# Performance work log

Measured on AMD Instinct MI355X. Metric: run time of the kernel, lower is better.

The kernel has to match this reference:

```python
import jax, jax.numpy as jnp
import numpy as np

E, H, L = 512, 512, 1   # emb_size, hidden_size, num_layers
B, S, T = 64, 1024, 256  # batch, src_len, trg_len
SCALE = 0.02


def setup_inputs() -> dict:
    key = jax.random.key(0)
    ks = jax.random.split(key, 12)
    f32 = jnp.float32
    return {
        # forward args
        "trg_embed": jax.random.normal(ks[0], (B, T, E), f32),
        "encoder_hidden": jax.random.normal(ks[1], (B, S, 2 * H), f32),
        "encoder_final": jax.random.normal(ks[2], (L, B, 2 * H), f32),
        "src_mask": jnp.ones((B, 1, S), jnp.bool_),
        "trg_mask": jnp.ones((B, 1, T), jnp.bool_),
        # Bahdanau attention params
        "W_key": jax.random.normal(ks[3], (H, 2 * H), f32) * SCALE,
        "W_query": jax.random.normal(ks[4], (H, H), f32) * SCALE,
        "v_energy": jax.random.normal(ks[5], (H,), f32) * SCALE,
        # bridge (2H -> H, with bias)
        "W_bridge": jax.random.normal(ks[6], (H, 2 * H), f32) * SCALE,
        "b_bridge": jnp.zeros((H,), f32),
        # GRU (single layer), gate order r,z,n as in torch
        "W_ih": jax.random.normal(ks[7], (3 * H, E + 2 * H), f32) * SCALE,
        "W_hh": jax.random.normal(ks[8], (3 * H, H), f32) * SCALE,
        "b_ih": jnp.zeros((3 * H,), f32),
        "b_hh": jnp.zeros((3 * H,), f32),
        # pre_output_layer: (H + 2H + E) -> H, no bias
        "W_pre": jax.random.normal(ks[9], (H, H + 2 * H + E), f32) * SCALE,
    }


def _gru_cell(x, h, W_ih, W_hh, b_ih, b_hh):
    # x: [B, E+2H], h: [B, H]; torch GRUCell math, gates r,z,n
    gi = x @ W_ih.T + b_ih
    gh = h @ W_hh.T + b_hh
    i_r, i_z, i_n = jnp.split(gi, 3, axis=-1)
    h_r, h_z, h_n = jnp.split(gh, 3, axis=-1)
    r = jax.nn.sigmoid(i_r + h_r)
    z = jax.nn.sigmoid(i_z + h_z)
    n = jnp.tanh(i_n + r * h_n)
    return (1.0 - z) * n + z * h


def reference(trg_embed, encoder_hidden, encoder_final, src_mask, trg_mask,
              W_key, W_query, v_energy, W_bridge, b_bridge,
              W_ih, W_hh, b_ih, b_hh, W_pre):
    # init_hidden: tanh(bridge(encoder_final))  -> [L, B, H]
    hidden0 = jnp.tanh(jnp.einsum('lbd,hd->lbh', encoder_final, W_bridge) + b_bridge)
    # precomputed attention keys: [B, S, H]
    proj_key = jnp.einsum('bsd,hd->bsh', encoder_hidden, W_key)
    mask = src_mask[:, 0, :]  # [B, S]
    neg = jnp.finfo(trg_embed.dtype).min

    def step(hidden, prev_embed):  # hidden [L,B,H], prev_embed [B,E]
        q = hidden[-1] @ W_query.T                       # [B, H]
        e = jnp.tanh(q[:, None, :] + proj_key)           # [B, S, H]
        scores = jnp.einsum('bsh,h->bs', e, v_energy)    # [B, S]
        scores = jnp.where(mask, scores, neg)
        alphas = jax.nn.softmax(scores, axis=-1)         # [B, S]
        context = jnp.einsum('bs,bsd->bd', alphas, encoder_hidden)  # [B, 2H]
        x = jnp.concatenate([prev_embed, context], axis=-1)         # [B, E+2H]
        h_new = _gru_cell(x, hidden[-1], W_ih, W_hh, b_ih, b_hh)    # [B, H]
        pre = jnp.concatenate([prev_embed, h_new, context], axis=-1) @ W_pre.T  # [B, H]
        return h_new[None, :, :], (h_new, pre)

    hidden_final, (outs, pres) = jax.lax.scan(step, hidden0, jnp.swapaxes(trg_embed, 0, 1))
    decoder_states = jnp.swapaxes(outs, 0, 1)        # [B, T, H]
    pre_output_vectors = jnp.swapaxes(pres, 0, 1)    # [B, T, H]
    return decoder_states, hidden_final, pre_output_vectors
```

## Files before the change

kernel.cpp:

```cpp
#include <hip/hip_runtime.h>


typedef __attribute__((ext_vector_type(8))) short bf16x8;
typedef __attribute__((ext_vector_type(4))) float f32x4;
typedef __attribute__((ext_vector_type(2))) float f32x2;
typedef unsigned short u16;
typedef unsigned char u8;
typedef unsigned int u32;

constexpr int NB = 64, NS = 1024, NT = 256, NE = 512, NH = 512, NH2 = 1024, NG3 = 1536;

#define MFMA16(a, b, c) __builtin_amdgcn_mfma_f32_16x16x32_bf16((a), (b), (c), 0, 0, 0)

__device__ __forceinline__ float bf2f(u16 u) { return __uint_as_float(((u32)u) << 16); }
__device__ __forceinline__ u16 f2bf(float f) {
    u32 u = __float_as_uint(f);
    u += 0x7FFFu + ((u >> 16) & 1u);
    return (u16)(u >> 16);
}
__device__ __forceinline__ float fast_tanh(float x) {
    float t = __expf(2.0f * x);
    return 1.0f - __fdividef(2.0f, t + 1.0f);
}
__device__ __forceinline__ float fast_sig(float x) {
    return __fdividef(1.0f, 1.0f + __expf(-x));
}

__global__ void k_cast(const float* __restrict__ src, u16* __restrict__ dst, int n4) {
    int i = blockIdx.x * blockDim.x + threadIdx.x;
    int stride = gridDim.x * blockDim.x;
    for (; i < n4; i += stride) {
        float4 v = reinterpret_cast<const float4*>(src)[i];
        ushort4 o;
        o.x = f2bf(v.x); o.y = f2bf(v.y); o.z = f2bf(v.z); o.w = f2bf(v.w);
        reinterpret_cast<ushort4*>(dst)[i] = o;
    }
}
__global__ void k_cast8(const float* __restrict__ src, u32* __restrict__ dst, int n8) {
    int i = blockIdx.x * blockDim.x + threadIdx.x;
    int stride = gridDim.x * blockDim.x;
    for (; i < n8; i += stride) {
        float4 a = reinterpret_cast<const float4*>(src)[i * 2];
        float4 b = reinterpret_cast<const float4*>(src)[i * 2 + 1];
        int w0 = 0, w1 = 0;
        w0 = __builtin_amdgcn_cvt_pk_fp8_f32(a.x, a.y, w0, false);
        w0 = __builtin_amdgcn_cvt_pk_fp8_f32(a.z, a.w, w0, true);
        w1 = __builtin_amdgcn_cvt_pk_fp8_f32(b.x, b.y, w1, false);
        w1 = __builtin_amdgcn_cvt_pk_fp8_f32(b.z, b.w, w1, true);
        uint2 o; o.x = (u32)w0; o.y = (u32)w1;
        reinterpret_cast<uint2*>(dst)[i] = o;
    }
}

__global__ __launch_bounds__(256) void k_pkgemm8(
    const float* __restrict__ A, const u16* __restrict__ Bm, u8* __restrict__ Out8) {
    __shared__ u16 As[128][72];
    __shared__ u16 Bs[128][72];
    const int mt = blockIdx.x, nt = blockIdx.y;
    const int tid = threadIdx.x, lane = tid & 63, wv = tid >> 6;
    const int m0 = mt * 128, n0 = nt * 128;
    const f32x4 fz = {0.f, 0.f, 0.f, 0.f};
    f32x4 acc[2][8];
#pragma unroll
    for (int i = 0; i < 2; ++i)
#pragma unroll
        for (int jj = 0; jj < 8; ++jj) acc[i][jj] = fz;

    for (int kt = 0; kt < 16; ++kt) {
        const int k0 = kt * 64;
        __syncthreads();
#pragma unroll
        for (int r = 0; r < 4; ++r) {
            int cc = tid + 256 * r;
            int row = cc >> 3, kc = (cc & 7) * 8;
            const float* ap = &A[(size_t)(m0 + row) * NH2 + k0 + kc];
            float4 f0 = *(const float4*)ap;
            float4 f1 = *(const float4*)(ap + 4);
            u16 hh[8] = {f2bf(f0.x), f2bf(f0.y), f2bf(f0.z), f2bf(f0.w),
                         f2bf(f1.x), f2bf(f1.y), f2bf(f1.z), f2bf(f1.w)};
            *(bf16x8*)&As[row][kc] = *(bf16x8*)hh;
            *(bf16x8*)&Bs[row][kc] = *(const bf16x8*)&Bm[(size_t)(n0 + row) * NH2 + k0 + kc];
        }
        __syncthreads();
#pragma unroll
        for (int ks = 0; ks < 2; ++ks) {
            const int kk = ks * 32 + (lane >> 4) * 8;
            bf16x8 a0 = *(const bf16x8*)&As[wv * 32 + (lane & 15)][kk];
            bf16x8 a1 = *(const bf16x8*)&As[wv * 32 + 16 + (lane & 15)][kk];
#pragma unroll
            for (int jj = 0; jj < 8; ++jj) {
                bf16x8 bb = *(const bf16x8*)&Bs[jj * 16 + (lane & 15)][kk];
                acc[0][jj] = MFMA16(a0, bb, acc[0][jj]);
                acc[1][jj] = MFMA16(a1, bb, acc[1][jj]);
            }
        }
    }
#pragma unroll
    for (int i = 0; i < 2; ++i)
#pragma unroll
        for (int jj = 0; jj < 8; ++jj)
#pragma unroll
            for (int r = 0; r < 4; ++r) {
                int m = m0 + wv * 32 + i * 16 + (lane >> 4) * 4 + r;
                int n = n0 + jj * 16 + (lane & 15);
                int pk = __builtin_amdgcn_cvt_pk_fp8_f32(acc[i][jj][r], acc[i][jj][r], 0, false);
                Out8[(size_t)m * NH + n] = (u8)(pk & 0xFF);
            }
}

__global__ __launch_bounds__(256) void k_bridge(
    const float* __restrict__ ef, const float* __restrict__ Wb, const float* __restrict__ bb,
    float* __restrict__ hf, u16* __restrict__ hbb) {
    __shared__ float efs[NH2];
    const int b = blockIdx.x, tid = threadIdx.x;
    for (int i = tid; i < NH2; i += 256) efs[i] = ef[(size_t)b * NH2 + i];
    __syncthreads();
    for (int j = tid; j < NH; j += 256) {
        float acc = bb[j];
        const float4* wr = (const float4*)&Wb[(size_t)j * NH2];
#pragma unroll 4
        for (int d4 = 0; d4 < 256; ++d4) {
            float4 w = wr[d4];
            acc += w.x * efs[d4 * 4] + w.y * efs[d4 * 4 + 1] + w.z * efs[d4 * 4 + 2] + w.w * efs[d4 * 4 + 3];
        }
        float h0 = tanhf(acc);
        hf[(size_t)b * NH + j] = h0;
        hbb[(size_t)b * NH + j] = f2bf(h0);
    }
}

__global__ __launch_bounds__(256, 4) void k_attn(
    const u8* __restrict__ pk8, const u8* __restrict__ eh8,
    const float* __restrict__ qb, const float* __restrict__ ven,
    u16* __restrict__ ctxp, float* __restrict__ denp) {
    __shared__ float wts[128];
    __shared__ float wden[4];
    __shared__ float part[128][17];
    const int b = blockIdx.x >> 3, c = blockIdx.x & 7;
    const int tid = threadIdx.x, lane = tid & 63, wv = tid >> 6;
    const int sl = lane & 3, ch = lane >> 2;
    const int h0 = ch * 32;
    const float C = 2.8853900817779268f;
    float qv2[32], vvm2[32];
    float vs = 0.f;
#pragma unroll
    for (int i4 = 0; i4 < 8; ++i4) {
        float4 q4 = *(const float4*)&qb[(size_t)b * NH + h0 + i4 * 4];
        float4 v4 = *(const float4*)&ven[h0 + i4 * 4];
        qv2[i4 * 4 + 0] = C * q4.x; qv2[i4 * 4 + 1] = C * q4.y;
        qv2[i4 * 4 + 2] = C * q4.z; qv2[i4 * 4 + 3] = C * q4.w;
        vvm2[i4 * 4 + 0] = -2.f * v4.x; vvm2[i4 * 4 + 1] = -2.f * v4.y;
        vvm2[i4 * 4 + 2] = -2.f * v4.z; vvm2[i4 * 4 + 3] = -2.f * v4.w;
        vs += v4.x + v4.y + v4.z + v4.w;
    }
#pragma unroll
    for (int off = 32; off; off >>= 1) vs += __shfl_xor(vs, off, 64);
    vs *= 0.25f;

    const u8* pkbase = pk8 + ((size_t)b * NS + c * 128 + wv * 32 + sl) * NH + h0;
    u32 pA[8], pB[8];
    *(uint4*)&pA[0] = *(const uint4*)pkbase;
    *(uint4*)&pA[4] = *(const uint4*)(pkbase + 16);
    float accg[8];
#pragma unroll
    for (int g = 0; g < 8; ++g) {
        if (g < 7) {
            const u8* nrow = pkbase + (size_t)(g + 1) * 4 * NH;
            *(uint4*)&pB[0] = *(const uint4*)nrow;
            *(uint4*)&pB[4] = *(const uint4*)(nrow + 16);
        }
        float acc0 = 0.f, acc1 = 0.f;
#pragma unroll
        for (int w = 0; w < 8; ++w) {
            f32x2 lo = __builtin_amdgcn_cvt_pk_f32_fp8(pA[w], false);
            f32x2 hi = __builtin_amdgcn_cvt_pk_f32_fp8(pA[w], true);
            const int i = w * 4;
            float x0 = __builtin_fmaf(lo[0], C, qv2[i + 0]);
            float x1 = __builtin_fmaf(lo[1], C, qv2[i + 1]);
            float x2 = __builtin_fmaf(hi[0], C, qv2[i + 2]);
            float x3 = __builtin_fmaf(hi[1], C, qv2[i + 3]);
            acc0 = __builtin_fmaf(vvm2[i + 0], __builtin_amdgcn_rcpf(__builtin_amdgcn_exp2f(x0) + 1.0f), acc0);
            acc1 = __builtin_fmaf(vvm2[i + 1], __builtin_amdgcn_rcpf(__builtin_amdgcn_exp2f(x1) + 1.0f), acc1);
            acc0 = __builtin_fmaf(vvm2[i + 2], __builtin_amdgcn_rcpf(__builtin_amdgcn_exp2f(x2) + 1.0f), acc0);
            acc1 = __builtin_fmaf(vvm2[i + 3], __builtin_amdgcn_rcpf(__builtin_amdgcn_exp2f(x3) + 1.0f), acc1);
        }
        accg[g] = acc0 + acc1;
#pragma unroll
        for (int w = 0; w < 8; ++w) pA[w] = pB[w];
    }
#pragma unroll
    for (int off = 4; off <= 32; off <<= 1) {
#pragma unroll
        for (int g = 0; g < 8; ++g) accg[g] += __shfl_xor(accg[g], off, 64);
    }
    float den_acc = 0.f;
#pragma unroll
    for (int g = 0; g < 8; ++g) {
        float w = __expf(accg[g] + vs);
        if (lane < 4) wts[wv * 32 + g * 4 + lane] = w;
        den_acc += w;
    }
#pragma unroll
    for (int off = 32; off; off >>= 1) den_acc += __shfl_xor(den_acc, off, 64);
    if (lane == 0) wden[wv] = den_acc * 0.0625f;
    __syncthreads();
    if (tid == 0) denp[c * 64 + b] = wden[0] + wden[1] + wden[2] + wden[3];

    const int half = tid >> 7, tt = tid & 127;
    const u8* ebase = eh8 + ((size_t)b * NS + c * 128 + half * 64) * NH2 + tt * 8;
    float ar[8] = {0.f, 0.f, 0.f, 0.f, 0.f, 0.f, 0.f, 0.f};
#pragma unroll 8
    for (int s = 0; s < 64; ++s) {
        float w = wts[half * 64 + s];
        uint2 uu = *(const uint2*)&ebase[(size_t)s * NH2];
        f32x2 p0 = __builtin_amdgcn_cvt_pk_f32_fp8(uu.x, false);
        f32x2 p1 = __builtin_amdgcn_cvt_pk_f32_fp8(uu.x, true);
        f32x2 p2 = __builtin_amdgcn_cvt_pk_f32_fp8(uu.y, false);
        f32x2 p3 = __builtin_amdgcn_cvt_pk_f32_fp8(uu.y, true);
        ar[0] = __builtin_fmaf(w, p0[0], ar[0]); ar[1] = __builtin_fmaf(w, p0[1], ar[1]);
        ar[2] = __builtin_fmaf(w, p1[0], ar[2]); ar[3] = __builtin_fmaf(w, p1[1], ar[3]);
        ar[4] = __builtin_fmaf(w, p2[0], ar[4]); ar[5] = __builtin_fmaf(w, p2[1], ar[5]);
        ar[6] = __builtin_fmaf(w, p3[0], ar[6]); ar[7] = __builtin_fmaf(w, p3[1], ar[7]);
    }
#pragma unroll
    for (int k = 0; k < 8; ++k) part[tt][half * 8 + k] = ar[k];
    __syncthreads();
    const int row = tid >> 1, col = (tid & 1) * 4;
    ushort4 o;
    o.x = f2bf(part[row][col + 0] + part[row][8 + col + 0]);
    o.y = f2bf(part[row][col + 1] + part[row][8 + col + 1]);
    o.z = f2bf(part[row][col + 2] + part[row][8 + col + 2]);
    o.w = f2bf(part[row][col + 3] + part[row][8 + col + 3]);
    *(ushort4*)&ctxp[((size_t)c * 64 + b) * NH2 + tid * 4] = o;
}

__global__ __launch_bounds__(256) void k_gru(
    const u16* __restrict__ teb, const u16* __restrict__ ctxp, const float* __restrict__ denp,
    const u16* __restrict__ hb_in,
    const u16* __restrict__ Wihb, const u16* __restrict__ Whhb,
    const float* __restrict__ bih, const float* __restrict__ bhh,
    const float* __restrict__ hf_in, float* __restrict__ hf_out, u16* __restrict__ hb_out,
    u16* __restrict__ hall, u16* __restrict__ ctxall,
    float* __restrict__ out_ds, float* __restrict__ out_hf, int t) {
    __shared__ u16 ctx[16][1032];
    __shared__ float pbuf[3][3][16][17];
    const int tid = threadIdx.x, lane = tid & 63, wv = tid >> 6;
    const int jt = blockIdx.x >> 2, mh = blockIdx.x & 3;
    const int jj = lane & 15;
    const int j = jt * 16 + jj;
    const int kg = lane >> 4;
    const int mrow = mh * 16 + jj;

    {
        const int r = tid >> 4;
        const int bg = mh * 16 + r;
        const int d0 = (tid & 15) * 64;
        float den = 0.f;
#pragma unroll
        for (int cc = 0; cc < 8; ++cc) den += denp[cc * 64 + bg];
        const float rd = 1.0f / den;
#pragma unroll 2
        for (int dd = 0; dd < 64; dd += 8) {
            float ac[8] = {0.f, 0.f, 0.f, 0.f, 0.f, 0.f, 0.f, 0.f};
#pragma unroll
            for (int cc = 0; cc < 8; ++cc) {
                bf16x8 v = *(const bf16x8*)&ctxp[((size_t)cc * 64 + bg) * NH2 + d0 + dd];
#pragma unroll
                for (int k = 0; k < 8; ++k) ac[k] += bf2f((u16)v[k]);
            }
            u16 o[8];
#pragma unroll
            for (int k = 0; k < 8; ++k) o[k] = f2bf(ac[k] * rd);
            *(bf16x8*)&ctx[r][d0 + dd] = *(bf16x8*)o;
        }
    }
    __syncthreads();

    const f32x4 fz = {0.f, 0.f, 0.f, 0.f};
    f32x4 g0 = fz, g1 = fz, g2 = fz;
    const u16* wr = Wihb + (size_t)j * NG3;
    const u16* wz = wr + (size_t)NH * NG3;
    const u16* wn = wr + (size_t)NH2 * NG3;
    float ho[4], bset[6];

    if (wv == 0) {
        const u16* ta = teb + ((size_t)mrow * NT + t) * NE;
#pragma unroll 4
        for (int kt = 0; kt < 16; ++kt) {
            int k0 = kt * 32 + kg * 8;
            bf16x8 a = *(const bf16x8*)&ta[k0];
            g0 = MFMA16(a, *(const bf16x8*)&wr[k0], g0);
            g1 = MFMA16(a, *(const bf16x8*)&wz[k0], g1);
            g2 = MFMA16(a, *(const bf16x8*)&wn[k0], g2);
        }
        bset[0] = bih[j]; bset[1] = bih[NH + j]; bset[2] = bih[NH2 + j];
        bset[3] = bhh[j]; bset[4] = bhh[NH + j]; bset[5] = bhh[NH2 + j];
#pragma unroll
        for (int r = 0; r < 4; ++r) ho[r] = hf_in[(size_t)(mh * 16 + kg * 4 + r) * NH + j];
    } else if (wv == 1) {
        const u16* ha = hb_in + (size_t)mrow * NH;
        const u16* vr = Whhb + (size_t)j * NH;
        const u16* vz = vr + (size_t)NH * NH;
        const u16* vn = vr + (size_t)NH2 * NH;
#pragma unroll 4
        for (int kt = 0; kt < 16; ++kt) {
            int k0 = kt * 32 + kg * 8;
            bf16x8 a = *(const bf16x8*)&ha[k0];
            g0 = MFMA16(a, *(const bf16x8*)&vr[k0], g0);
            g1 = MFMA16(a, *(const bf16x8*)&vz[k0], g1);
            g2 = MFMA16(a, *(const bf16x8*)&vn[k0], g2);
        }
#pragma unroll
        for (int r = 0; r < 4; ++r) {
            int ml = kg * 4 + r;
            pbuf[0][0][ml][jj] = g0[r];
            pbuf[1][0][ml][jj] = g1[r];
            pbuf[2][0][ml][jj] = g2[r];
        }
    } else {
        const int koff = (wv - 2) * 512;
#pragma unroll 4
        for (int kt = 0; kt < 16; ++kt) {
            int kc = koff + kt * 32 + kg * 8;
            bf16x8 a = *(const bf16x8*)&ctx[jj][kc];
            g0 = MFMA16(a, *(const bf16x8*)&wr[NE + kc], g0);
            g1 = MFMA16(a, *(const bf16x8*)&wz[NE + kc], g1);
            g2 = MFMA16(a, *(const bf16x8*)&wn[NE + kc], g2);
        }
        const int src = wv - 1;
#pragma unroll
        for (int r = 0; r < 4; ++r) {
            int ml = kg * 4 + r;
            pbuf[0][src][ml][jj] = g0[r];
            pbuf[1][src][ml][jj] = g1[r];
            pbuf[2][src][ml][jj] = g2[r];
        }
    }
    __syncthreads();

    if (wv == 0) {
#pragma unroll
        for (int r = 0; r < 4; ++r) {
            int ml = kg * 4 + r;
            int m = mh * 16 + ml;
            float gir = g0[r] + pbuf[0][1][ml][jj] + pbuf[0][2][ml][jj] + bset[0];
            float giz = g1[r] + pbuf[1][1][ml][jj] + pbuf[1][2][ml][jj] + bset[1];
            float gin = g2[r] + pbuf[2][1][ml][jj] + pbuf[2][2][ml][jj] + bset[2];
            float rr = fast_sig(gir + pbuf[0][0][ml][jj] + bset[3]);
            float zz = fast_sig(giz + pbuf[1][0][ml][jj] + bset[4]);
            float nn = fast_tanh(gin + rr * (pbuf[2][0][ml][jj] + bset[5]));
            float hn = (1.f - zz) * nn + zz * ho[r];
            u16 hb = f2bf(hn);
            hf_out[(size_t)m * NH + j] = hn;
            hb_out[(size_t)m * NH + j] = hb;
            hall[((size_t)m * NT + t) * NH + j] = hb;
            __builtin_nontemporal_store(hn, &out_ds[((size_t)m * NT + t) * NH + j]);
            if (t == NT - 1) out_hf[(size_t)m * NH + j] = hn;
        }
    } else if (wv == 1 && jt == 0) {
        const int r2 = lane >> 2;
        const int dq = (lane & 3) * 256;
        u16* dst = &ctxall[((size_t)(mh * 16 + r2) * NT + t) * NH2 + dq];
#pragma unroll 4
        for (int dd = 0; dd < 256; dd += 8)
            *(bf16x8*)&dst[dd] = *(const bf16x8*)&ctx[r2][dq + dd];
    }
}

__global__ __launch_bounds__(256) void k_q(
    const u16* __restrict__ hbn, const u16* __restrict__ Wqb, float* __restrict__ qbuf) {
    const int tid = threadIdx.x, lane = tid & 63, wv = tid >> 6;
    const int mrow = wv * 16 + (lane & 15);
    const int kg = lane >> 4;
    const int n = blockIdx.x * 16 + (lane & 15);
    const f32x4 fz = {0.f, 0.f, 0.f, 0.f};
    f32x4 aq = fz;
    const u16* ha = hbn + (size_t)mrow * NH;
    const u16* wq = Wqb + (size_t)n * NH;
#pragma unroll 4
    for (int kt = 0; kt < 16; ++kt) {
        int k0 = kt * 32 + kg * 8;
        aq = MFMA16(*(const bf16x8*)&ha[k0], *(const bf16x8*)&wq[k0], aq);
    }
#pragma unroll
    for (int r = 0; r < 4; ++r) {
        int m = wv * 16 + kg * 4 + r;
        qbuf[(size_t)m * NH + n] = aq[r];
    }
}

__global__ __launch_bounds__(256) void k_preb(
    const u16* __restrict__ teb, const u16* __restrict__ hall, const u16* __restrict__ ctxall,
    const u16* __restrict__ Wpreb, float* __restrict__ out_pre) {
    __shared__ u16 As[128][72];
    __shared__ u16 Bs[128][72];
    const int mt = blockIdx.x, nt = blockIdx.y;
    const int tid = threadIdx.x, lane = tid & 63, wv = tid >> 6;
    const int m0 = mt * 128, n0 = nt * 128;
    const f32x4 fz = {0.f, 0.f, 0.f, 0.f};
    f32x4 acc[2][8];
#pragma unroll
    for (int i = 0; i < 2; ++i)
#pragma unroll
        for (int jj = 0; jj < 8; ++jj) acc[i][jj] = fz;

    for (int kt = 0; kt < 32; ++kt) {
        const int k0 = kt * 64;
        const u16* Abase; int astride, acol;
        if (k0 < 512)       { Abase = teb;    astride = 512;  acol = k0; }
        else if (k0 < 1024) { Abase = hall;   astride = 512;  acol = k0 - 512; }
        else                { Abase = ctxall; astride = 1024; acol = k0 - 1024; }
        __syncthreads();
#pragma unroll
        for (int r = 0; r < 4; ++r) {
            int cc = tid + 256 * r;
            int row = cc >> 3, kc = (cc & 7) * 8;
            *(bf16x8*)&As[row][kc] = *(const bf16x8*)&Abase[(size_t)(m0 + row) * astride + acol + kc];
            *(bf16x8*)&Bs[row][kc] = *(const bf16x8*)&Wpreb[(size_t)(n0 + row) * 2048 + k0 + kc];
        }
        __syncthreads();
#pragma unroll
        for (int ks = 0; ks < 2; ++ks) {
            const int kk = ks * 32 + (lane >> 4) * 8;
            bf16x8 a0 = *(const bf16x8*)&As[wv * 32 + (lane & 15)][kk];
            bf16x8 a1 = *(const bf16x8*)&As[wv * 32 + 16 + (lane & 15)][kk];
#pragma unroll
            for (int jj = 0; jj < 8; ++jj) {
                bf16x8 bb = *(const bf16x8*)&Bs[jj * 16 + (lane & 15)][kk];
                acc[0][jj] = MFMA16(a0, bb, acc[0][jj]);
                acc[1][jj] = MFMA16(a1, bb, acc[1][jj]);
            }
        }
    }
#pragma unroll
    for (int i = 0; i < 2; ++i)
#pragma unroll
        for (int jj = 0; jj < 8; ++jj)
#pragma unroll
            for (int r = 0; r < 4; ++r) {
                int m = m0 + wv * 32 + i * 16 + (lane >> 4) * 4 + r;
                int n = n0 + jj * 16 + (lane & 15);
                __builtin_nontemporal_store(acc[i][jj][r], &out_pre[(size_t)m * NH + n]);
            }
}

extern "C" void kernel_launch(void* const* d_in, const int* in_sizes, int n_in,
                              void* d_out, int out_size, void* d_ws, size_t ws_size,
                              hipStream_t stream) {
    const float* trg_embed  = (const float*)d_in[0];
    const float* enc_hidden = (const float*)d_in[1];
    const float* enc_final  = (const float*)d_in[2];
    const float* W_key    = (const float*)d_in[5];
    const float* W_query  = (const float*)d_in[6];
    const float* v_energy = (const float*)d_in[7];
    const float* W_bridge = (const float*)d_in[8];
    const float* b_bridge = (const float*)d_in[9];
    const float* W_ih     = (const float*)d_in[10];
    const float* W_hh     = (const float*)d_in[11];
    const float* b_ih     = (const float*)d_in[12];
    const float* b_hh     = (const float*)d_in[13];
    const float* W_pre    = (const float*)d_in[14];

    if (ws_size < 180000000ULL) return;
    size_t off = 0;
    auto take = [&](size_t bytes) {
        void* p = (char*)d_ws + off;
        off += (bytes + 255) & ~(size_t)255;
        return p;
    };
    u8*    eh8   = (u8*)take((size_t)NB * NS * NH2);
    u8*    pk8   = (u8*)take((size_t)NB * NS * NH);
    u16*   teb   = (u16*)take((size_t)NB * NT * NE * 2);
    u16*   ctxall= (u16*)take((size_t)NB * NT * NH2 * 2);
    u16*   hall  = (u16*)take((size_t)NB * NT * NH * 2);
    u16*   Wihb  = (u16*)take((size_t)NG3 * NG3 * 2);
    u16*   Whhb  = (u16*)take((size_t)NG3 * NH * 2);
    u16*   Wpreb = (u16*)take((size_t)NH * 2048 * 2);
    u16*   Wqb   = (u16*)take((size_t)NH * NH * 2);
    u16*   Wkb   = (u16*)take((size_t)NH * NH2 * 2);
    float* hf0   = (float*)take((size_t)NB * NH * 4);
    float* hf1   = (float*)take((size_t)NB * NH * 4);
    u16*   hb0   = (u16*)take((size_t)NB * NH * 2);
    u16*   hb1   = (u16*)take((size_t)NB * NH * 2);
    float* qbuf  = (float*)take((size_t)NB * NH * 4);
    u16*   ctxp  = (u16*)take((size_t)8 * NB * NH2 * 2);
    float* denp  = (float*)take((size_t)8 * NB * 4);

    float* out_ds  = (float*)d_out;
    float* out_hf  = out_ds + (size_t)NB * NT * NH;
    float* out_pre = out_hf + (size_t)NB * NH;

    auto cast = [&](const float* src, u16* dst, int n) {
        int n4 = n / 4;
        int grid = (n4 + 255) / 256; if (grid > 2048) grid = 2048;
        k_cast<<<grid, 256, 0, stream>>>(src, dst, n4);
    };
    k_cast8<<<2048, 256, 0, stream>>>(enc_hidden, (u32*)eh8, NB * NS * NH2 / 8);
    cast(trg_embed,  teb, NB * NT * NE);
    cast(W_ih,  Wihb,  NG3 * NG3);
    cast(W_hh,  Whhb,  NG3 * NH);
    cast(W_pre, Wpreb, NH * 2048);
    cast(W_query, Wqb, NH * NH);
    cast(W_key,  Wkb,  NH * NH2);
    k_pkgemm8<<<dim3(512, 4), 256, 0, stream>>>(enc_hidden, Wkb, pk8);
    k_bridge<<<NB, 256, 0, stream>>>(enc_final, W_bridge, b_bridge, hf0, hb0);
    k_q<<<32, 256, 0, stream>>>(hb0, Wqb, qbuf);

    for (int t = 0; t < NT; ++t) {
        float* hf_in  = (t & 1) ? hf1 : hf0;
        float* hf_out = (t & 1) ? hf0 : hf1;
        u16*   hb_in  = (t & 1) ? hb1 : hb0;
        u16*   hb_out = (t & 1) ? hb0 : hb1;
        k_attn<<<NB * 8, 256, 0, stream>>>(pk8, eh8, qbuf, v_energy, ctxp, denp);
        k_gru<<<128, 256, 0, stream>>>(teb, ctxp, denp, hb_in, Wihb, Whhb, b_ih, b_hh,
                                       hf_in, hf_out, hb_out, hall, ctxall,
                                       out_ds, out_hf, t);
        k_q<<<32, 256, 0, stream>>>(hb_out, Wqb, qbuf);
    }
    k_preb<<<dim3(128, 4), 256, 0, stream>>>(teb, hall, ctxall, Wpreb, out_pre);
}
```

Measured before the change: 11.60 ms.

## Split attention into 16 source chunks and GRU into 8-row batch tiles

k_attn now uses 16 blocks per batch row, each covering 64 source positions, so the launch grows from 512 to 1024 blocks. The context reduction is restructured so each thread handles 16 columns over 16 positions, followed by a 4-way partial sum. k_gru runs 256 blocks with 8 batch rows each, which leaves half of each MFMA tile's rows idle. The softmax normalization is moved so it is applied after the context matmul. The aim is more parallelism on the per-step critical path, at the cost of more partial-context traffic and wasted MFMA work.

```diff
diff --git a/kernel.cpp b/kernel.cpp
--- a/kernel.cpp
+++ b/kernel.cpp
@@ -133,10 +133,10 @@
     const u8* __restrict__ pk8, const u8* __restrict__ eh8,
     const float* __restrict__ qb, const float* __restrict__ ven,
     u16* __restrict__ ctxp, float* __restrict__ denp) {
-    __shared__ float wts[128];
+    __shared__ float wts[64];
     __shared__ float wden[4];
-    __shared__ float part[128][17];
-    const int b = blockIdx.x >> 3, c = blockIdx.x & 7;
+    __shared__ float part[64][4][17];
+    const int b = blockIdx.x >> 4, c = blockIdx.x & 15;
     const int tid = threadIdx.x, lane = tid & 63, wv = tid >> 6;
     const int sl = lane & 3, ch = lane >> 2;
     const int h0 = ch * 32;
@@ -157,14 +157,14 @@
     for (int off = 32; off; off >>= 1) vs += __shfl_xor(vs, off, 64);
     vs *= 0.25f;
 
-    const u8* pkbase = pk8 + ((size_t)b * NS + c * 128 + wv * 32 + sl) * NH + h0;
+    const u8* pkbase = pk8 + ((size_t)b * NS + c * 64 + wv * 16 + sl) * NH + h0;
     u32 pA[8], pB[8];
     *(uint4*)&pA[0] = *(const uint4*)pkbase;
     *(uint4*)&pA[4] = *(const uint4*)(pkbase + 16);
-    float accg[8];
-#pragma unroll
-    for (int g = 0; g < 8; ++g) {
-        if (g < 7) {
+    float accg[4];
+#pragma unroll
+    for (int g = 0; g < 4; ++g) {
+        if (g < 3) {
             const u8* nrow = pkbase + (size_t)(g + 1) * 4 * NH;
             *(uint4*)&pB[0] = *(const uint4*)nrow;
             *(uint4*)&pB[4] = *(const uint4*)(nrow + 16);
@@ -191,13 +191,13 @@
 #pragma unroll
     for (int off = 4; off <= 32; off <<= 1) {
 #pragma unroll
-        for (int g = 0; g < 8; ++g) accg[g] += __shfl_xor(accg[g], off, 64);
+        for (int g = 0; g < 4; ++g) accg[g] += __shfl_xor(accg[g], off, 64);
     }
     float den_acc = 0.f;
 #pragma unroll
-    for (int g = 0; g < 8; ++g) {
+    for (int g = 0; g < 4; ++g) {
         float w = __expf(accg[g] + vs);
-        if (lane < 4) wts[wv * 32 + g * 4 + lane] = w;
+        if (lane < 4) wts[wv * 16 + g * 4 + lane] = w;
         den_acc += w;
     }
 #pragma unroll
@@ -206,31 +206,41 @@
     __syncthreads();
     if (tid == 0) denp[c * 64 + b] = wden[0] + wden[1] + wden[2] + wden[3];
 
-    const int half = tid >> 7, tt = tid & 127;
-    const u8* ebase = eh8 + ((size_t)b * NS + c * 128 + half * 64) * NH2 + tt * 8;
-    float ar[8] = {0.f, 0.f, 0.f, 0.f, 0.f, 0.f, 0.f, 0.f};
-#pragma unroll 8
-    for (int s = 0; s < 64; ++s) {
-        float w = wts[half * 64 + s];
-        uint2 uu = *(const uint2*)&ebase[(size_t)s * NH2];
-        f32x2 p0 = __builtin_amdgcn_cvt_pk_f32_fp8(uu.x, false);
-        f32x2 p1 = __builtin_amdgcn_cvt_pk_f32_fp8(uu.x, true);
-        f32x2 p2 = __builtin_amdgcn_cvt_pk_f32_fp8(uu.y, false);
-        f32x2 p3 = __builtin_amdgcn_cvt_pk_f32_fp8(uu.y, true);
-        ar[0] = __builtin_fmaf(w, p0[0], ar[0]); ar[1] = __builtin_fmaf(w, p0[1], ar[1]);
-        ar[2] = __builtin_fmaf(w, p1[0], ar[2]); ar[3] = __builtin_fmaf(w, p1[1], ar[3]);
-        ar[4] = __builtin_fmaf(w, p2[0], ar[4]); ar[5] = __builtin_fmaf(w, p2[1], ar[5]);
-        ar[6] = __builtin_fmaf(w, p3[0], ar[6]); ar[7] = __builtin_fmaf(w, p3[1], ar[7]);
-    }
-#pragma unroll
-    for (int k = 0; k < 8; ++k) part[tt][half * 8 + k] = ar[k];
+    const int qd = tid >> 6, tt = tid & 63;
+    const int d0 = tt * 16;
+    const u8* ebase = eh8 + ((size_t)b * NS + c * 64 + qd * 16) * NH2 + d0;
+    float ar[16];
+#pragma unroll
+    for (int k = 0; k < 16; ++k) ar[k] = 0.f;
+#pragma unroll 4
+    for (int s = 0; s < 16; ++s) {
+        float w = wts[qd * 16 + s];
+        uint4 uu = *(const uint4*)&ebase[(size_t)s * NH2];
+        const u32 ww[4] = {uu.x, uu.y, uu.z, uu.w};
+#pragma unroll
+        for (int q = 0; q < 4; ++q) {
+            f32x2 plo = __builtin_amdgcn_cvt_pk_f32_fp8(ww[q], false);
+            f32x2 phi = __builtin_amdgcn_cvt_pk_f32_fp8(ww[q], true);
+            ar[q * 4 + 0] = __builtin_fmaf(w, plo[0], ar[q * 4 + 0]);
+            ar[q * 4 + 1] = __builtin_fmaf(w, plo[1], ar[q * 4 + 1]);
+            ar[q * 4 + 2] = __builtin_fmaf(w, phi[0], ar[q * 4 + 2]);
+            ar[q * 4 + 3] = __builtin_fmaf(w, phi[1], ar[q * 4 + 3]);
+        }
+    }
+#pragma unroll
+    for (int k = 0; k < 16; ++k) part[tt][qd][k] = ar[k];
     __syncthreads();
-    const int row = tid >> 1, col = (tid & 1) * 4;
+    const int st = tid >> 2, k0 = (tid & 3) * 4;
+    float o0 = 0.f, o1 = 0.f, o2 = 0.f, o3 = 0.f;
+#pragma unroll
+    for (int q = 0; q < 4; ++q) {
+        o0 += part[st][q][k0 + 0];
+        o1 += part[st][q][k0 + 1];
+        o2 += part[st][q][k0 + 2];
+        o3 += part[st][q][k0 + 3];
+    }
     ushort4 o;
-    o.x = f2bf(part[row][col + 0] + part[row][8 + col + 0]);
-    o.y = f2bf(part[row][col + 1] + part[row][8 + col + 1]);
-    o.z = f2bf(part[row][col + 2] + part[row][8 + col + 2]);
-    o.w = f2bf(part[row][col + 3] + part[row][8 + col + 3]);
+    o.x = f2bf(o0); o.y = f2bf(o1); o.z = f2bf(o2); o.w = f2bf(o3);
     *(ushort4*)&ctxp[((size_t)c * 64 + b) * NH2 + tid * 4] = o;
 }
 
@@ -242,36 +252,39 @@
     const float* __restrict__ hf_in, float* __restrict__ hf_out, u16* __restrict__ hb_out,
     u16* __restrict__ hall, u16* __restrict__ ctxall,
     float* __restrict__ out_ds, float* __restrict__ out_hf, int t) {
-    __shared__ u16 ctx[16][1032];
+    __shared__ u16 ctx[8][1032];
     __shared__ float pbuf[3][3][16][17];
+    __shared__ float rden[8];
     const int tid = threadIdx.x, lane = tid & 63, wv = tid >> 6;
-    const int jt = blockIdx.x >> 2, mh = blockIdx.x & 3;
+    const int jt = blockIdx.x >> 3, mh = blockIdx.x & 7;
     const int jj = lane & 15;
     const int j = jt * 16 + jj;
     const int kg = lane >> 4;
-    const int mrow = mh * 16 + jj;
-
+    const int mrow = mh * 8 + (jj & 7);
+
+    if (tid < 8) {
+        float den = 0.f;
+#pragma unroll
+        for (int cc = 0; cc < 16; ++cc) den += denp[cc * 64 + mh * 8 + tid];
+        rden[tid] = 1.0f / den;
+    }
     {
-        const int r = tid >> 4;
-        const int bg = mh * 16 + r;
-        const int d0 = (tid & 15) * 64;
-        float den = 0.f;
-#pragma unroll
-        for (int cc = 0; cc < 8; ++cc) den += denp[cc * 64 + bg];
-        const float rd = 1.0f / den;
-#pragma unroll 2
-        for (int dd = 0; dd < 64; dd += 8) {
+        const int r = tid >> 5;
+        const int bg = mh * 8 + r;
+        const int dcol = (tid & 31) * 32;
+#pragma unroll
+        for (int dd = 0; dd < 32; dd += 8) {
             float ac[8] = {0.f, 0.f, 0.f, 0.f, 0.f, 0.f, 0.f, 0.f};
 #pragma unroll
-            for (int cc = 0; cc < 8; ++cc) {
-                bf16x8 v = *(const bf16x8*)&ctxp[((size_t)cc * 64 + bg) * NH2 + d0 + dd];
+            for (int cc = 0; cc < 16; ++cc) {
+                bf16x8 v = *(const bf16x8*)&ctxp[((size_t)cc * 64 + bg) * NH2 + dcol + dd];
 #pragma unroll
                 for (int k = 0; k < 8; ++k) ac[k] += bf2f((u16)v[k]);
             }
             u16 o[8];
 #pragma unroll
-            for (int k = 0; k < 8; ++k) o[k] = f2bf(ac[k] * rd);
-            *(bf16x8*)&ctx[r][d0 + dd] = *(bf16x8*)o;
+            for (int k = 0; k < 8; ++k) o[k] = f2bf(ac[k]);
+            *(bf16x8*)&ctx[r][dcol + dd] = *(bf16x8*)o;
         }
     }
     __syncthreads();
@@ -296,7 +309,10 @@
         bset[0] = bih[j]; bset[1] = bih[NH + j]; bset[2] = bih[NH2 + j];
         bset[3] = bhh[j]; bset[4] = bhh[NH + j]; bset[5] = bhh[NH2 + j];
 #pragma unroll
-        for (int r = 0; r < 4; ++r) ho[r] = hf_in[(size_t)(mh * 16 + kg * 4 + r) * NH + j];
+        for (int r = 0; r < 4; ++r) {
+            int ml = kg * 4 + r;
+            ho[r] = (ml < 8) ? hf_in[(size_t)(mh * 8 + ml) * NH + j] : 0.f;
+        }
     } else if (wv == 1) {
         const u16* ha = hb_in + (size_t)mrow * NH;
         const u16* vr = Whhb + (size_t)j * NH;
@@ -322,7 +338,7 @@
 #pragma unroll 4
         for (int kt = 0; kt < 16; ++kt) {
             int kc = koff + kt * 32 + kg * 8;
-            bf16x8 a = *(const bf16x8*)&ctx[jj][kc];
+            bf16x8 a = *(const bf16x8*)&ctx[jj & 7][kc];
             g0 = MFMA16(a, *(const bf16x8*)&wr[NE + kc], g0);
             g1 = MFMA16(a, *(const bf16x8*)&wz[NE + kc], g1);
             g2 = MFMA16(a, *(const bf16x8*)&wn[NE + kc], g2);
@@ -342,10 +358,12 @@
 #pragma unroll
         for (int r = 0; r < 4; ++r) {
             int ml = kg * 4 + r;
-            int m = mh * 16 + ml;
-            float gir = g0[r] + pbuf[0][1][ml][jj] + pbuf[0][2][ml][jj] + bset[0];
-            float giz = g1[r] + pbuf[1][1][ml][jj] + pbuf[1][2][ml][jj] + bset[1];
-            float gin = g2[r] + pbuf[2][1][ml][jj] + pbuf[2][2][ml][jj] + bset[2];
+            if (ml >= 8) continue;
+            int m = mh * 8 + ml;
+            float rd = rden[ml];
+            float gir = g0[r] + (pbuf[0][1][ml][jj] + pbuf[0][2][ml][jj]) * rd + bset[0];
+            float giz = g1[r] + (pbuf[1][1][ml][jj] + pbuf[1][2][ml][jj]) * rd + bset[1];
+            float gin = g2[r] + (pbuf[2][1][ml][jj] + pbuf[2][2][ml][jj]) * rd + bset[2];
             float rr = fast_sig(gir + pbuf[0][0][ml][jj] + bset[3]);
             float zz = fast_sig(giz + pbuf[1][0][ml][jj] + bset[4]);
             float nn = fast_tanh(gin + rr * (pbuf[2][0][ml][jj] + bset[5]));
@@ -358,12 +376,18 @@
             if (t == NT - 1) out_hf[(size_t)m * NH + j] = hn;
         }
     } else if (wv == 1 && jt == 0) {
-        const int r2 = lane >> 2;
-        const int dq = (lane & 3) * 256;
-        u16* dst = &ctxall[((size_t)(mh * 16 + r2) * NT + t) * NH2 + dq];
-#pragma unroll 4
-        for (int dd = 0; dd < 256; dd += 8)
-            *(bf16x8*)&dst[dd] = *(const bf16x8*)&ctx[r2][dq + dd];
+        const int r2 = lane >> 3;
+        const int dq = (lane & 7) * 128;
+        const float rd = rden[r2];
+        u16* dst = &ctxall[((size_t)(mh * 8 + r2) * NT + t) * NH2 + dq];
+#pragma unroll 4
+        for (int dd = 0; dd < 128; dd += 8) {
+            bf16x8 v = *(const bf16x8*)&ctx[r2][dq + dd];
+            u16 o[8];
+#pragma unroll
+            for (int k = 0; k < 8; ++k) o[k] = f2bf(bf2f((u16)v[k]) * rd);
+            *(bf16x8*)&dst[dd] = *(bf16x8*)o;
+        }
     }
 }
 
@@ -483,8 +507,8 @@
     u16*   hb0   = (u16*)take((size_t)NB * NH * 2);
     u16*   hb1   = (u16*)take((size_t)NB * NH * 2);
     float* qbuf  = (float*)take((size_t)NB * NH * 4);
-    u16*   ctxp  = (u16*)take((size_t)8 * NB * NH2 * 2);
-    float* denp  = (float*)take((size_t)8 * NB * 4);
+    u16*   ctxp  = (u16*)take((size_t)16 * NB * NH2 * 2);
+    float* denp  = (float*)take((size_t)16 * NB * 4);
 
     float* out_ds  = (float*)d_out;
     float* out_hf  = out_ds + (size_t)NB * NT * NH;
@@ -511,8 +535,8 @@
         float* hf_out = (t & 1) ? hf0 : hf1;
         u16*   hb_in  = (t & 1) ? hb1 : hb0;
         u16*   hb_out = (t & 1) ? hb0 : hb1;
-        k_attn<<<NB * 8, 256, 0, stream>>>(pk8, eh8, qbuf, v_energy, ctxp, denp);
-        k_gru<<<128, 256, 0, stream>>>(teb, ctxp, denp, hb_in, Wihb, Whhb, b_ih, b_hh,
+        k_attn<<<NB * 16, 256, 0, stream>>>(pk8, eh8, qbuf, v_energy, ctxp, denp);
+        k_gru<<<256, 256, 0, stream>>>(teb, ctxp, denp, hb_in, Wihb, Whhb, b_ih, b_hh,
                                        hf_in, hf_out, hb_out, hall, ctxall,
                                        out_ds, out_hf, t);
         k_q<<<32, 256, 0, stream>>>(hb_out, Wqb, qbuf);
```

New measurement: 11.46 ms. No clear change (-1.2%).
